# Kernel optimization log

Measured on AMD Instinct MI355X. Metric: run time of the kernel, lower is better.

Reference implementation:

```python
import jax, jax.numpy as jnp
import numpy as np

# Static graph / model sizes (closed over; match input_specs)
N0, N1, N2 = 500_000, 100_000, 25_000   # nodes per hop (targets are prefix of sources)
E0, E1 = 1_600_000, 400_000             # edges per hop
D_IN, D_H, D_OUT = 128, 256, 128


def setup_inputs() -> dict:
    key = jax.random.key(0)
    ks = jax.random.split(key, 11)
    s_in = 1.0 / np.sqrt(D_IN)
    s_h = 1.0 / np.sqrt(D_H)
    return {
        "x": jax.random.normal(ks[0], (N0, D_IN), dtype=jnp.float32),
        # layer 0 params (SAGEConv in->hidden): lin_l (with bias) on aggregated, lin_r (no bias) on root
        "W_l0": jax.random.normal(ks[1], (D_H, D_IN), dtype=jnp.float32) * s_in,
        "b_l0": jax.random.normal(ks[2], (D_H,), dtype=jnp.float32) * s_in,
        "W_r0": jax.random.normal(ks[3], (D_H, D_IN), dtype=jnp.float32) * s_in,
        # layer 1 params (SAGEConv hidden->out)
        "W_l1": jax.random.normal(ks[4], (D_OUT, D_H), dtype=jnp.float32) * s_h,
        "b_l1": jax.random.normal(ks[5], (D_OUT,), dtype=jnp.float32) * s_h,
        "W_r1": jax.random.normal(ks[6], (D_OUT, D_H), dtype=jnp.float32) * s_h,
        # bipartite edge indices: src in [0, N_src), dst in [0, N_dst)
        "ei0_src": jax.random.randint(ks[7], (E0,), 0, N0),
        "ei0_dst": jax.random.randint(ks[8], (E0,), 0, N1),
        "ei1_src": jax.random.randint(ks[9], (E1,), 0, N1),
        "ei1_dst": jax.random.randint(ks[10], (E1,), 0, N2),
    }


def _sage_conv(x_src, x_dst, src, dst, n_dst, W_l, b_l, W_r):
    """PyG SAGEConv, aggr='mean': lin_l(mean_neigh) + lin_r(x_dst)."""
    msg = x_src[src]                                                # [E, d] gather
    agg = jax.ops.segment_sum(msg, dst, num_segments=n_dst)        # [n_dst, d]
    cnt = jax.ops.segment_sum(jnp.ones((src.shape[0],), msg.dtype), dst,
                              num_segments=n_dst)                  # [n_dst]
    agg = agg / jnp.clip(cnt, 1.0)[:, None]                        # mean (safe for isolated nodes)
    return agg @ W_l.T + b_l + x_dst @ W_r.T


def reference(x, W_l0, b_l0, W_r0, W_l1, b_l1, W_r1,
              ei0_src, ei0_dst, ei1_src, ei1_dst):
    # hop 0: targets are first N1 rows of x
    h = _sage_conv(x, x[:N1], ei0_src, ei0_dst, N1, W_l0, b_l0, W_r0)
    h = jax.nn.relu(h)  # relu on all but last layer
    # hop 1 (last layer, no relu)
    out = _sage_conv(h, h[:N2], ei1_src, ei1_dst, N2, W_l1, b_l1, W_r1)
    return out
```

## Files before the change

kernel.cpp:

```cpp
#include <hip/hip_runtime.h>
#include <hip/hip_bf16.h>

#define cN0 500000
#define cN1 100000
#define cN2 25000
#define cE0 1600000
#define cE1 400000

typedef __bf16 bf16x8 __attribute__((ext_vector_type(8)));
typedef __bf16 bf16x4 __attribute__((ext_vector_type(4)));
typedef float f32x4 __attribute__((ext_vector_type(4)));


__global__ void k_hist(const int* __restrict__ dst, int E, int* __restrict__ cnt) {
    int i = blockIdx.x * blockDim.x + threadIdx.x;
    if (i < E) atomicAdd(&cnt[dst[i]], 1);
}

__global__ void k_scan1(int* __restrict__ a, int n, int* __restrict__ bsum) {
    __shared__ int lds[256];
    const int t = threadIdx.x;
    const int base = blockIdx.x * 1024 + t * 4;
    int v0 = (base + 0 < n) ? a[base + 0] : 0;
    int v1 = (base + 1 < n) ? a[base + 1] : 0;
    int v2 = (base + 2 < n) ? a[base + 2] : 0;
    int v3 = (base + 3 < n) ? a[base + 3] : 0;
    const int s = v0 + v1 + v2 + v3;
    lds[t] = s;
    __syncthreads();
    int x = s;
    for (int d = 1; d < 256; d <<= 1) {
        int y = (t >= d) ? lds[t - d] : 0;
        __syncthreads();
        x += y;
        lds[t] = x;
        __syncthreads();
    }
    if (t == 255) bsum[blockIdx.x] = x;
    int e0 = x - s;
    int e1 = e0 + v0, e2 = e1 + v1, e3 = e2 + v2;
    if (base + 0 < n) a[base + 0] = e0;
    if (base + 1 < n) a[base + 1] = e1;
    if (base + 2 < n) a[base + 2] = e2;
    if (base + 3 < n) a[base + 3] = e3;
}

__global__ void k_scan2(int* __restrict__ bsum, int nb) {
    __shared__ int lds[128];
    const int t = threadIdx.x;
    int v = (t < nb) ? bsum[t] : 0;
    lds[t] = v;
    __syncthreads();
    int x = v;
    for (int d = 1; d < 128; d <<= 1) {
        int y = (t >= d) ? lds[t - d] : 0;
        __syncthreads();
        x += y;
        lds[t] = x;
        __syncthreads();
    }
    if (t < nb) bsum[t] = x - v;
}

__global__ void k_scan3(int* __restrict__ a, int n, const int* __restrict__ bsum, int total,
                        int* __restrict__ cur) {
    int i = blockIdx.x * blockDim.x + threadIdx.x;
    if (i < n) {
        int v = a[i] + bsum[i >> 10];
        a[i] = v;
        cur[i] = v;
    }
    if (i == 0) a[n] = total;
}

__global__ void k_scatter(const int* __restrict__ esrc, const int* __restrict__ edst, int E,
                          int* __restrict__ cur, int* __restrict__ srcs) {
    int i = blockIdx.x * blockDim.x + threadIdx.x;
    if (i < E) {
        int p = atomicAdd(&cur[edst[i]], 1);
        srcs[p] = esrc[i];
    }
}

__global__ __launch_bounds__(256) void k_cast(const float* __restrict__ x,
                                              __bf16* __restrict__ xb, int n8) {
    int i = blockIdx.x * blockDim.x + threadIdx.x;
    if (i < n8) {
        const float4 v0 = *(const float4*)(x + (size_t)i * 8);
        const float4 v1 = *(const float4*)(x + (size_t)i * 8 + 4);
        bf16x8 o;
        o[0] = (__bf16)v0.x; o[1] = (__bf16)v0.y; o[2] = (__bf16)v0.z; o[3] = (__bf16)v0.w;
        o[4] = (__bf16)v1.x; o[5] = (__bf16)v1.y; o[6] = (__bf16)v1.z; o[7] = (__bf16)v1.w;
        *(bf16x8*)(xb + (size_t)i * 8) = o;
    }
}

__global__ void k_wcat0(const float* __restrict__ Wl, const float* __restrict__ Wr,
                        __bf16* __restrict__ Wc) {
    int i = blockIdx.x * blockDim.x + threadIdx.x;
    if (i < 256 * 256) {
        int j = i >> 8, k = i & 255;
        float v = (k < 128) ? Wl[j * 128 + k] : Wr[j * 128 + (k - 128)];
        Wc[i] = (__bf16)v;
    }
}
__global__ void k_wcat1(const float* __restrict__ Wl, const float* __restrict__ Wr,
                        __bf16* __restrict__ Wc) {
    int i = blockIdx.x * blockDim.x + threadIdx.x;
    if (i < 128 * 512) {
        int j = i >> 9, k = i & 511;
        float v = (k < 256) ? Wl[j * 256 + k] : Wr[j * 256 + (k - 256)];
        Wc[i] = (__bf16)v;
    }
}

__global__ __launch_bounds__(256) void k_agg0(
    const __bf16* __restrict__ xb,
    const int* __restrict__ off, const int* __restrict__ srcs,
    const __bf16* __restrict__ zrow,
    __bf16* __restrict__ Agg)
{
    const int wid = blockIdx.x * 4 + (threadIdx.x >> 6);
    const int lane = threadIdx.x & 63;
    const int slot = lane >> 4;
    const int dl = lane & 15;
    const int gbase = wid * 8;
    for (int n = 0; n < 8; ++n) {
        const int g = gbase + n;
        if (g >= cN1) return;
        const int e0 = off[g], e1 = off[g + 1];
        const int deg = e1 - e0;
        float a[8] = {0.f, 0.f, 0.f, 0.f, 0.f, 0.f, 0.f, 0.f};
        const int iters = (deg + 3) >> 2;
        for (int it = 0; it < iters; ++it) {
            const int e = e0 + it * 4 + slot;
            const __bf16* rp = zrow;
            if (e < e1) rp = xb + (size_t)srcs[e] * 128;
            const bf16x8 r = *(const bf16x8*)(rp + dl * 8);
            #pragma unroll
            for (int d = 0; d < 8; ++d) a[d] += (float)r[d];
        }
        #pragma unroll
        for (int d = 0; d < 8; ++d) {
            a[d] += __shfl_xor(a[d], 16);
            a[d] += __shfl_xor(a[d], 32);
        }
        if (slot == 0) {
            const float inv = 1.f / (float)(deg > 0 ? deg : 1);
            bf16x8 o;
            #pragma unroll
            for (int d = 0; d < 8; ++d) o[d] = (__bf16)(a[d] * inv);
            *(bf16x8*)(Agg + (size_t)g * 128 + dl * 8) = o;
        }
    }
}

__global__ __launch_bounds__(256) void k_agg1(
    const __bf16* __restrict__ h,
    const int* __restrict__ off, const int* __restrict__ srcs,
    const __bf16* __restrict__ zrow,
    __bf16* __restrict__ Agg)
{
    const int wid = blockIdx.x * 4 + (threadIdx.x >> 6);
    const int lane = threadIdx.x & 63;
    const int slot = lane >> 5;
    const int dl = lane & 31;
    const int gbase = wid * 4;
    for (int n = 0; n < 4; ++n) {
        const int g = gbase + n;
        if (g >= cN2) return;
        const int e0 = off[g], e1 = off[g + 1];
        const int deg = e1 - e0;
        float a[8] = {0.f, 0.f, 0.f, 0.f, 0.f, 0.f, 0.f, 0.f};
        const int iters = (deg + 1) >> 1;
        for (int it = 0; it < iters; ++it) {
            const int e = e0 + it * 2 + slot;
            const __bf16* rp = zrow;
            if (e < e1) rp = h + (size_t)srcs[e] * 256;
            const bf16x8 r = *(const bf16x8*)(rp + dl * 8);
            #pragma unroll
            for (int d = 0; d < 8; ++d) a[d] += (float)r[d];
        }
        #pragma unroll
        for (int d = 0; d < 8; ++d) a[d] += __shfl_xor(a[d], 32);
        if (slot == 0) {
            const float inv = 1.f / (float)(deg > 0 ? deg : 1);
            bf16x8 o;
            #pragma unroll
            for (int d = 0; d < 8; ++d) o[d] = (__bf16)(a[d] * inv);
            *(bf16x8*)(Agg + (size_t)g * 256 + dl * 8) = o;
        }
    }
}

template<int KHALF, int LDC, bool RELU, bool OUTBF16>
__global__ __launch_bounds__(256) void k_gemm(
    const __bf16* __restrict__ A1, const __bf16* __restrict__ A2,
    const __bf16* __restrict__ W, const float* __restrict__ bias,
    float* __restrict__ outf, __bf16* __restrict__ outb, int Mrows)
{
    const int K = KHALF * 2;
    const int tid = threadIdx.x;
    const int l = tid & 63;
    const int w = tid >> 6;
    const int wm = w & 1, wn = w >> 1;
    const int row0 = blockIdx.x * 128 + wm * 64;
    const int col0 = blockIdx.y * 128 + wn * 64;
    const int lr = l & 15;
    const int lk = (l >> 4) * 8;

    const __bf16* pa1[4];
    const __bf16* pa2[4];
    const __bf16* pb[4];
    #pragma unroll
    for (int i = 0; i < 4; ++i) {
        int r = row0 + i * 16 + lr;
        r = (r < Mrows) ? r : (Mrows - 1);
        pa1[i] = A1 + (size_t)r * KHALF + lk;
        pa2[i] = A2 + (size_t)r * KHALF + lk;
        pb[i] = W + (size_t)(col0 + i * 16 + lr) * K + lk;
    }
    f32x4 acc[4][4];
    #pragma unroll
    for (int i = 0; i < 4; ++i)
        #pragma unroll
        for (int j = 0; j < 4; ++j)
            acc[i][j] = (f32x4)0.0f;

    #pragma unroll 2
    for (int k0 = 0; k0 < KHALF; k0 += 32) {
        bf16x8 fa[4], fb[4];
        #pragma unroll
        for (int i = 0; i < 4; ++i) fa[i] = *(const bf16x8*)(pa1[i] + k0);
        #pragma unroll
        for (int j = 0; j < 4; ++j) fb[j] = *(const bf16x8*)(pb[j] + k0);
        #pragma unroll
        for (int i = 0; i < 4; ++i)
            #pragma unroll
            for (int j = 0; j < 4; ++j)
                acc[i][j] = __builtin_amdgcn_mfma_f32_16x16x32_bf16(fa[i], fb[j], acc[i][j], 0, 0, 0);
    }
    #pragma unroll 2
    for (int k0 = 0; k0 < KHALF; k0 += 32) {
        bf16x8 fa[4], fb[4];
        #pragma unroll
        for (int i = 0; i < 4; ++i) fa[i] = *(const bf16x8*)(pa2[i] + k0);
        #pragma unroll
        for (int j = 0; j < 4; ++j) fb[j] = *(const bf16x8*)(pb[j] + KHALF + k0);
        #pragma unroll
        for (int i = 0; i < 4; ++i)
            #pragma unroll
            for (int j = 0; j < 4; ++j)
                acc[i][j] = __builtin_amdgcn_mfma_f32_16x16x32_bf16(fa[i], fb[j], acc[i][j], 0, 0, 0);
    }

    #pragma unroll
    for (int j = 0; j < 4; ++j) {
        const int colg = col0 + j * 16 + lr;
        const float bj = bias[colg];
        #pragma unroll
        for (int i = 0; i < 4; ++i) {
            #pragma unroll
            for (int reg = 0; reg < 4; ++reg) {
                const int rowg = row0 + i * 16 + (l >> 4) * 4 + reg;
                if (rowg < Mrows) {
                    float v = acc[i][j][reg] + bj;
                    if (RELU) v = fmaxf(v, 0.f);
                    if (OUTBF16) outb[(size_t)rowg * LDC + colg] = (__bf16)v;
                    else         outf[(size_t)rowg * LDC + colg] = v;
                }
            }
        }
    }
}


extern "C" void kernel_launch(void* const* d_in, const int* in_sizes, int n_in,
                              void* d_out, int out_size, void* d_ws, size_t ws_size,
                              hipStream_t stream) {
    const float* x   = (const float*)d_in[0];
    const float* Wl0 = (const float*)d_in[1];
    const float* bl0 = (const float*)d_in[2];
    const float* Wr0 = (const float*)d_in[3];
    const float* Wl1 = (const float*)d_in[4];
    const float* bl1 = (const float*)d_in[5];
    const float* Wr1 = (const float*)d_in[6];
    const int* e0s = (const int*)d_in[7];
    const int* e0d = (const int*)d_in[8];
    const int* e1s = (const int*)d_in[9];
    const int* e1d = (const int*)d_in[10];
    float* out = (float*)d_out;

    char* ws = (char*)d_ws;
    size_t pos = 0;
    auto alloc = [&](size_t nb) -> void* {
        void* p = ws + pos;
        pos += (nb + 255) & ~(size_t)255;
        return p;
    };
    __bf16* xb   = (__bf16*)alloc((size_t)cN0 * 128 * 2);
    __bf16* h    = (__bf16*)alloc((size_t)cN1 * 256 * 2);
    __bf16* Agg0 = (__bf16*)alloc((size_t)cN1 * 128 * 2);
    __bf16* Agg1 = Agg0;
    int* off0    = (int*)alloc((size_t)(cN1 + 1) * 4);
    int* cur0    = (int*)alloc((size_t)cN1 * 4);
    int* srcs0   = (int*)alloc((size_t)cE0 * 4);
    int* off1    = (int*)alloc((size_t)(cN2 + 1) * 4);
    int* cur1    = (int*)alloc((size_t)cN2 * 4);
    int* srcs1   = (int*)alloc((size_t)cE1 * 4);
    int* bsum    = (int*)alloc(128 * 4);
    __bf16* Wc0  = (__bf16*)alloc(256 * 256 * 2);
    __bf16* Wc1  = (__bf16*)alloc(128 * 512 * 2);
    __bf16* zrow = (__bf16*)alloc(256 * 2);
    (void)ws_size; (void)in_sizes; (void)n_in; (void)out_size;

    hipMemsetAsync(off0, 0, (size_t)(cN1 + 1) * 4, stream);
    hipMemsetAsync(off1, 0, (size_t)(cN2 + 1) * 4, stream);
    hipMemsetAsync(zrow, 0, 256 * 2, stream);
    k_cast<<<(cN0 * 128 / 8 + 255) / 256, 256, 0, stream>>>(x, xb, cN0 * 128 / 8);

    k_hist<<<(cE0 + 255) / 256, 256, 0, stream>>>(e0d, cE0, off0);
    k_hist<<<(cE1 + 255) / 256, 256, 0, stream>>>(e1d, cE1, off1);

    const int nb0 = (cN1 + 1023) / 1024;
    k_scan1<<<nb0, 256, 0, stream>>>(off0, cN1, bsum);
    k_scan2<<<1, 128, 0, stream>>>(bsum, nb0);
    k_scan3<<<(cN1 + 255) / 256, 256, 0, stream>>>(off0, cN1, bsum, cE0, cur0);
    k_scatter<<<(cE0 + 255) / 256, 256, 0, stream>>>(e0s, e0d, cE0, cur0, srcs0);

    const int nb1 = (cN2 + 1023) / 1024;
    k_scan1<<<nb1, 256, 0, stream>>>(off1, cN2, bsum);
    k_scan2<<<1, 128, 0, stream>>>(bsum, nb1);
    k_scan3<<<(cN2 + 255) / 256, 256, 0, stream>>>(off1, cN2, bsum, cE1, cur1);
    k_scatter<<<(cE1 + 255) / 256, 256, 0, stream>>>(e1s, e1d, cE1, cur1, srcs1);

    k_wcat0<<<(256 * 256 + 255) / 256, 256, 0, stream>>>(Wl0, Wr0, Wc0);
    k_wcat1<<<(128 * 512 + 255) / 256, 256, 0, stream>>>(Wl1, Wr1, Wc1);

    k_agg0<<<(cN1 + 31) / 32, 256, 0, stream>>>(xb, off0, srcs0, zrow, Agg0);
    {
        dim3 grid((cN1 + 127) / 128, 2);
        k_gemm<128, 256, true, true><<<grid, 256, 0, stream>>>(Agg0, xb, Wc0, bl0, nullptr, h, cN1);
    }
    k_agg1<<<(cN2 + 15) / 16, 256, 0, stream>>>(h, off1, srcs1, zrow, Agg1);
    {
        dim3 grid((cN2 + 127) / 128, 1);
        k_gemm<256, 128, false, false><<<grid, 256, 0, stream>>>(Agg1, h, Wc1, bl1, out, nullptr, cN2);
    }
}
```

Baseline: 879.4 us.

## Fuse preprocessing launches into combined cast/hist/weight, scan and scatter kernels

Merges the input cast, both edge histograms and both weight concatenations into one block-partitioned kernel. The two CSR scans and the two scatters are likewise batched into single launches, and the three memsets become one by placing the offsets and zero row contiguously. This cuts about fourteen small launches down to five, removing launch gaps and letting independent work for the two hops overlap. The cost is more complex block-index dispatch with hardcoded block counts.

```diff
diff --git a/kernel.cpp b/kernel.cpp
--- a/kernel.cpp
+++ b/kernel.cpp
@@ -11,16 +11,50 @@
 typedef __bf16 bf16x4 __attribute__((ext_vector_type(4)));
 typedef float f32x4 __attribute__((ext_vector_type(4)));
 
-
-__global__ void k_hist(const int* __restrict__ dst, int E, int* __restrict__ cnt) {
-    int i = blockIdx.x * blockDim.x + threadIdx.x;
-    if (i < E) atomicAdd(&cnt[dst[i]], 1);
-}
-
-__global__ void k_scan1(int* __restrict__ a, int n, int* __restrict__ bsum) {
+__global__ __launch_bounds__(256) void k_prep(
+    const float* __restrict__ x, __bf16* __restrict__ xb,
+    const int* __restrict__ e0d, int* __restrict__ off0,
+    const int* __restrict__ e1d, int* __restrict__ off1,
+    const float* __restrict__ Wl0, const float* __restrict__ Wr0, __bf16* __restrict__ Wc0,
+    const float* __restrict__ Wl1, const float* __restrict__ Wr1, __bf16* __restrict__ Wc1)
+{
+    const int b = blockIdx.x;
+    const int t = threadIdx.x;
+    if (b < 31250) {
+        const int i = b * 256 + t;
+        const float4 v0 = *(const float4*)(x + (size_t)i * 8);
+        const float4 v1 = *(const float4*)(x + (size_t)i * 8 + 4);
+        bf16x8 o;
+        o[0] = (__bf16)v0.x; o[1] = (__bf16)v0.y; o[2] = (__bf16)v0.z; o[3] = (__bf16)v0.w;
+        o[4] = (__bf16)v1.x; o[5] = (__bf16)v1.y; o[6] = (__bf16)v1.z; o[7] = (__bf16)v1.w;
+        *(bf16x8*)(xb + (size_t)i * 8) = o;
+    } else if (b < 37500) {
+        const int i = (b - 31250) * 256 + t;
+        atomicAdd(&off0[e0d[i]], 1);
+    } else if (b < 39063) {
+        const int i = (b - 37500) * 256 + t;
+        if (i < cE1) atomicAdd(&off1[e1d[i]], 1);
+    } else if (b < 39319) {
+        const int i = (b - 39063) * 256 + t;
+        const int j = i >> 8, k = i & 255;
+        float v = (k < 128) ? Wl0[j * 128 + k] : Wr0[j * 128 + (k - 128)];
+        Wc0[i] = (__bf16)v;
+    } else {
+        const int i = (b - 39319) * 256 + t;
+        const int j = i >> 9, k = i & 511;
+        float v = (k < 256) ? Wl1[j * 256 + k] : Wr1[j * 256 + (k - 256)];
+        Wc1[i] = (__bf16)v;
+    }
+}
+
+__global__ void k_scanA(int* __restrict__ off0, int* __restrict__ bsum0,
+                        int* __restrict__ off1, int* __restrict__ bsum1) {
     __shared__ int lds[256];
     const int t = threadIdx.x;
-    const int base = blockIdx.x * 1024 + t * 4;
+    int* a; int n; int* bsum; int blk;
+    if (blockIdx.x < 98) { a = off0; n = cN1; bsum = bsum0; blk = blockIdx.x; }
+    else                 { a = off1; n = cN2; bsum = bsum1; blk = blockIdx.x - 98; }
+    const int base = blk * 1024 + t * 4;
     int v0 = (base + 0 < n) ? a[base + 0] : 0;
     int v1 = (base + 1 < n) ? a[base + 1] : 0;
     int v2 = (base + 2 < n) ? a[base + 2] : 0;
@@ -36,7 +70,7 @@
         lds[t] = x;
         __syncthreads();
     }
-    if (t == 255) bsum[blockIdx.x] = x;
+    if (t == 255) bsum[blk] = x;
     int e0 = x - s;
     int e1 = e0 + v0, e2 = e1 + v1, e3 = e2 + v2;
     if (base + 0 < n) a[base + 0] = e0;
@@ -45,9 +79,11 @@
     if (base + 3 < n) a[base + 3] = e3;
 }
 
-__global__ void k_scan2(int* __restrict__ bsum, int nb) {
+__global__ void k_scanB(int* __restrict__ bsum0, int* __restrict__ bsum1) {
     __shared__ int lds[128];
     const int t = threadIdx.x;
+    int* bsum = (blockIdx.x == 0) ? bsum0 : bsum1;
+    const int nb = (blockIdx.x == 0) ? 98 : 25;
     int v = (t < nb) ? bsum[t] : 0;
     lds[t] = v;
     __syncthreads();
@@ -62,9 +98,12 @@
     if (t < nb) bsum[t] = x - v;
 }
 
-__global__ void k_scan3(int* __restrict__ a, int n, const int* __restrict__ bsum, int total,
-                        int* __restrict__ cur) {
-    int i = blockIdx.x * blockDim.x + threadIdx.x;
+__global__ void k_scanC(int* __restrict__ off0, const int* __restrict__ bsum0, int* __restrict__ cur0,
+                        int* __restrict__ off1, const int* __restrict__ bsum1, int* __restrict__ cur1) {
+    int* a; const int* bsum; int* cur; int n, total, blk;
+    if (blockIdx.x < 391) { a = off0; bsum = bsum0; cur = cur0; n = cN1; total = cE0; blk = blockIdx.x; }
+    else                  { a = off1; bsum = bsum1; cur = cur1; n = cN2; total = cE1; blk = blockIdx.x - 391; }
+    const int i = blk * 256 + threadIdx.x;
     if (i < n) {
         int v = a[i] + bsum[i >> 10];
         a[i] = v;
@@ -73,44 +112,20 @@
     if (i == 0) a[n] = total;
 }
 
-__global__ void k_scatter(const int* __restrict__ esrc, const int* __restrict__ edst, int E,
-                          int* __restrict__ cur, int* __restrict__ srcs) {
-    int i = blockIdx.x * blockDim.x + threadIdx.x;
-    if (i < E) {
-        int p = atomicAdd(&cur[edst[i]], 1);
-        srcs[p] = esrc[i];
-    }
-}
-
-__global__ __launch_bounds__(256) void k_cast(const float* __restrict__ x,
-                                              __bf16* __restrict__ xb, int n8) {
-    int i = blockIdx.x * blockDim.x + threadIdx.x;
-    if (i < n8) {
-        const float4 v0 = *(const float4*)(x + (size_t)i * 8);
-        const float4 v1 = *(const float4*)(x + (size_t)i * 8 + 4);
-        bf16x8 o;
-        o[0] = (__bf16)v0.x; o[1] = (__bf16)v0.y; o[2] = (__bf16)v0.z; o[3] = (__bf16)v0.w;
-        o[4] = (__bf16)v1.x; o[5] = (__bf16)v1.y; o[6] = (__bf16)v1.z; o[7] = (__bf16)v1.w;
-        *(bf16x8*)(xb + (size_t)i * 8) = o;
-    }
-}
-
-__global__ void k_wcat0(const float* __restrict__ Wl, const float* __restrict__ Wr,
-                        __bf16* __restrict__ Wc) {
-    int i = blockIdx.x * blockDim.x + threadIdx.x;
-    if (i < 256 * 256) {
-        int j = i >> 8, k = i & 255;
-        float v = (k < 128) ? Wl[j * 128 + k] : Wr[j * 128 + (k - 128)];
-        Wc[i] = (__bf16)v;
-    }
-}
-__global__ void k_wcat1(const float* __restrict__ Wl, const float* __restrict__ Wr,
-                        __bf16* __restrict__ Wc) {
-    int i = blockIdx.x * blockDim.x + threadIdx.x;
-    if (i < 128 * 512) {
-        int j = i >> 9, k = i & 511;
-        float v = (k < 256) ? Wl[j * 256 + k] : Wr[j * 256 + (k - 256)];
-        Wc[i] = (__bf16)v;
+__global__ void k_scatter2(const int* __restrict__ e0s, const int* __restrict__ e0d,
+                           int* __restrict__ cur0, int* __restrict__ srcs0,
+                           const int* __restrict__ e1s, const int* __restrict__ e1d,
+                           int* __restrict__ cur1, int* __restrict__ srcs1) {
+    if (blockIdx.x < 6250) {
+        const int i = blockIdx.x * 256 + threadIdx.x;
+        const int p = atomicAdd(&cur0[e0d[i]], 1);
+        srcs0[p] = e0s[i];
+    } else {
+        const int i = (blockIdx.x - 6250) * 256 + threadIdx.x;
+        if (i < cE1) {
+            const int p = atomicAdd(&cur1[e1d[i]], 1);
+            srcs1[p] = e1s[i];
+        }
     }
 }
 
@@ -302,40 +317,27 @@
     __bf16* h    = (__bf16*)alloc((size_t)cN1 * 256 * 2);
     __bf16* Agg0 = (__bf16*)alloc((size_t)cN1 * 128 * 2);
     __bf16* Agg1 = Agg0;
-    int* off0    = (int*)alloc((size_t)(cN1 + 1) * 4);
+    int* off0    = (int*)alloc(((size_t)(cN1 + 1) + (cN2 + 1) + 128) * 4);
+    int* off1    = off0 + (cN1 + 1);
+    __bf16* zrow = (__bf16*)(off1 + (cN2 + 1));
+    const size_t zbytes = ((size_t)(cN1 + 1) + (cN2 + 1) + 128) * 4;
     int* cur0    = (int*)alloc((size_t)cN1 * 4);
     int* srcs0   = (int*)alloc((size_t)cE0 * 4);
-    int* off1    = (int*)alloc((size_t)(cN2 + 1) * 4);
     int* cur1    = (int*)alloc((size_t)cN2 * 4);
     int* srcs1   = (int*)alloc((size_t)cE1 * 4);
-    int* bsum    = (int*)alloc(128 * 4);
+    int* bsum0   = (int*)alloc(128 * 4);
+    int* bsum1   = (int*)alloc(128 * 4);
     __bf16* Wc0  = (__bf16*)alloc(256 * 256 * 2);
     __bf16* Wc1  = (__bf16*)alloc(128 * 512 * 2);
-    __bf16* zrow = (__bf16*)alloc(256 * 2);
     (void)ws_size; (void)in_sizes; (void)n_in; (void)out_size;
 
-    hipMemsetAsync(off0, 0, (size_t)(cN1 + 1) * 4, stream);
-    hipMemsetAsync(off1, 0, (size_t)(cN2 + 1) * 4, stream);
-    hipMemsetAsync(zrow, 0, 256 * 2, stream);
-    k_cast<<<(cN0 * 128 / 8 + 255) / 256, 256, 0, stream>>>(x, xb, cN0 * 128 / 8);
-
-    k_hist<<<(cE0 + 255) / 256, 256, 0, stream>>>(e0d, cE0, off0);
-    k_hist<<<(cE1 + 255) / 256, 256, 0, stream>>>(e1d, cE1, off1);
-
-    const int nb0 = (cN1 + 1023) / 1024;
-    k_scan1<<<nb0, 256, 0, stream>>>(off0, cN1, bsum);
-    k_scan2<<<1, 128, 0, stream>>>(bsum, nb0);
-    k_scan3<<<(cN1 + 255) / 256, 256, 0, stream>>>(off0, cN1, bsum, cE0, cur0);
-    k_scatter<<<(cE0 + 255) / 256, 256, 0, stream>>>(e0s, e0d, cE0, cur0, srcs0);
-
-    const int nb1 = (cN2 + 1023) / 1024;
-    k_scan1<<<nb1, 256, 0, stream>>>(off1, cN2, bsum);
-    k_scan2<<<1, 128, 0, stream>>>(bsum, nb1);
-    k_scan3<<<(cN2 + 255) / 256, 256, 0, stream>>>(off1, cN2, bsum, cE1, cur1);
-    k_scatter<<<(cE1 + 255) / 256, 256, 0, stream>>>(e1s, e1d, cE1, cur1, srcs1);
-
-    k_wcat0<<<(256 * 256 + 255) / 256, 256, 0, stream>>>(Wl0, Wr0, Wc0);
-    k_wcat1<<<(128 * 512 + 255) / 256, 256, 0, stream>>>(Wl1, Wr1, Wc1);
+    hipMemsetAsync(off0, 0, zbytes, stream);
+    k_prep<<<39575, 256, 0, stream>>>(x, xb, e0d, off0, e1d, off1,
+                                      Wl0, Wr0, Wc0, Wl1, Wr1, Wc1);
+    k_scanA<<<123, 256, 0, stream>>>(off0, bsum0, off1, bsum1);
+    k_scanB<<<2, 128, 0, stream>>>(bsum0, bsum1);
+    k_scanC<<<489, 256, 0, stream>>>(off0, bsum0, cur0, off1, bsum1, cur1);
+    k_scatter2<<<7813, 256, 0, stream>>>(e0s, e0d, cur0, srcs0, e1s, e1d, cur1, srcs1);
 
     k_agg0<<<(cN1 + 31) / 32, 256, 0, stream>>>(xb, off0, srcs0, zrow, Agg0);
     {
```

Result: faster. 850.5 us (-3.3%).
